# Optimization experiments

Measured on AMD Instinct MI355X. Metric: run time of the kernel, lower is better.

Reference implementation:

```python
import jax, jax.numpy as jnp
import numpy as np

EPS_SN = 1e-12
EPS_BN = 1e-5
NEG_SLOPE = 0.01  # nn.LeakyReLU default


def _l2n(v):
    return v / (jnp.linalg.norm(v) + EPS_SN)


def _sn_weight(w, u, v):
    # one power iteration (as in SpectralNorm._update_u_v), u/v are buffers
    h = w.shape[0]
    W2 = w.reshape(h, -1)
    Wd = jax.lax.stop_gradient(W2)
    v = _l2n(Wd.T @ u)
    u = _l2n(Wd @ v)
    sigma = u @ (W2 @ v)  # gradient flows through W2 only
    return w / sigma


def _conv(x, w, pad):
    return jax.lax.conv_general_dilated(
        x, w, window_strides=(1, 1), padding=[(pad, pad), (pad, pad)],
        dimension_numbers=('NCHW', 'OIHW', 'NCHW'))


def _bn(x, scale, bias):
    # BatchNorm2d in training mode: biased batch stats over (B,H,W)
    mean = x.mean(axis=(0, 2, 3), keepdims=True)
    var = x.var(axis=(0, 2, 3), keepdims=True)
    xn = (x - mean) * jax.lax.rsqrt(var + EPS_BN)
    return xn * scale[None, :, None, None] + bias[None, :, None, None]


def setup_inputs() -> dict:
    key = jax.random.key(0)
    ks = jax.random.split(key, 16)
    B, C, W, H = 2, 256, 64, 64
    Cq = C // 4
    inp = {
        'x': jax.random.normal(ks[0], (B, C, W, H), jnp.float32),
        'pre': jax.random.normal(ks[1], (B, C, W, H), jnp.float32),
        'mask': (jax.random.uniform(ks[2], (B, 1, W, H)) > 0.5).astype(jnp.float32),
        'q_w': jax.random.normal(ks[3], (Cq, C, 1, 1), jnp.float32) * 0.02,
        'gamma': jnp.array(0.5, jnp.float32),
        'alpha': jnp.array(0.5, jnp.float32),
        'bn1_s': jnp.ones((2 * C,), jnp.float32),
        'bn1_b': jnp.zeros((2 * C,), jnp.float32),
        'c1_w': jax.random.normal(ks[4], (C, 2 * C, 3, 3), jnp.float32) * 0.02,
        'u1': _l2n(jax.random.normal(ks[5], (C,), jnp.float32)),
        'v1': _l2n(jax.random.normal(ks[6], (2 * C * 9,), jnp.float32)),
        'bn2_s': jnp.ones((C,), jnp.float32),
        'bn2_b': jnp.zeros((C,), jnp.float32),
        'c2_w': jax.random.normal(ks[7], (C, C, 3, 3), jnp.float32) * 0.02,
        'u2': _l2n(jax.random.normal(ks[8], (C,), jnp.float32)),
        'v2': _l2n(jax.random.normal(ks[9], (C * 9,), jnp.float32)),
        'by_w': jax.random.normal(ks[10], (C, 2 * C, 1, 1), jnp.float32) * 0.02,
        'u3': _l2n(jax.random.normal(ks[11], (C,), jnp.float32)),
        'v3': _l2n(jax.random.normal(ks[12], (2 * C,), jnp.float32)),
    }
    return inp


def reference(x, pre, mask, q_w, gamma, alpha, bn1_s, bn1_b, c1_w, u1, v1,
              bn2_s, bn2_b, c2_w, u2, v2, by_w, u3, v3):
    B, C, W, H = x.shape
    N = W * H
    q = _conv(x, q_w, 0).reshape(B, -1, N)
    energy = jnp.einsum('bcn,bcm->bnm', q, q)       # B x N x N (query == key)
    attention = jax.nn.softmax(energy, axis=-1)
    val = x.reshape(B, C, N)
    # torch.bmm(value, attention^T): out[b,c,j] = sum_k val[b,c,k] * attn[b,j,k]
    out = jnp.einsum('bck,bjk->bcj', val, attention).reshape(B, C, W, H)
    out = gamma * out + x

    context_flow = jnp.einsum('bck,bjk->bcj', pre.reshape(B, -1, N), attention)
    context_flow = context_flow.reshape(B, -1, W, H)
    context_flow = alpha * (1 - mask) * context_flow + mask * pre

    y = jnp.concatenate([out, context_flow], axis=1)  # B x 2C x W x H
    # ResBlock(2C -> C, hidden C, BatchNorm, spectral norm, sample_type='none')
    h = jax.nn.leaky_relu(_bn(y, bn1_s, bn1_b), NEG_SLOPE)
    h = _conv(h, _sn_weight(c1_w, u1, v1), 1)
    h = jax.nn.leaky_relu(_bn(h, bn2_s, bn2_b), NEG_SLOPE)
    h = _conv(h, _sn_weight(c2_w, u2, v2), 1)
    sc = _conv(y, _sn_weight(by_w, u3, v3), 0)
    res = h + sc
    return res, attention
```

## Files before the change

### kernel.cpp

```cpp
#include <hip/hip_runtime.h>
#include <cstddef>


typedef __attribute__((ext_vector_type(8))) short bh8;
typedef __attribute__((ext_vector_type(4))) short bh4;
typedef __attribute__((ext_vector_type(4))) float f4;

static __device__ __forceinline__ short f2bf(float f) {
  unsigned u = __float_as_uint(f);
  unsigned r = (u + 0x7fffu + ((u >> 16) & 1u)) >> 16;
  return (short)r;
}
static __device__ __forceinline__ float bf2f(unsigned short s) {
  return __uint_as_float(((unsigned)s) << 16);
}

__device__ __forceinline__ float blk_sum256(float v, float* sm) {
#pragma unroll
  for (int o = 32; o > 0; o >>= 1) v += __shfl_down(v, o, 64);
  __syncthreads();
  if ((threadIdx.x & 63) == 0) sm[threadIdx.x >> 6] = v;
  __syncthreads();
  return sm[0] + sm[1] + sm[2] + sm[3];
}

__device__ __forceinline__ float blk_max256(float v, float* sm) {
#pragma unroll
  for (int o = 32; o > 0; o >>= 1) v = fmaxf(v, __shfl_down(v, o, 64));
  __syncthreads();
  if ((threadIdx.x & 63) == 0) sm[threadIdx.x >> 6] = v;
  __syncthreads();
  return fmaxf(fmaxf(sm[0], sm[1]), fmaxf(sm[2], sm[3]));
}

#define SWCOL(row, col) ((col) ^ ((((row) >> 1) & 3) << 3))

__global__ __launch_bounds__(256) void snA_kernel(
    const float* __restrict__ w1, const float* __restrict__ u1,
    const float* __restrict__ w2, const float* __restrict__ u2,
    const float* __restrict__ w3, const float* __restrict__ u3,
    float* __restrict__ t1, float* __restrict__ t2, float* __restrict__ t3) {
  int g = blockIdx.x * 256 + threadIdx.x;
  const float* W; const float* u; float* t; int K; int j;
  if (g < 4608)      { W = w1; u = u1; t = t1; K = 4608; j = g; }
  else if (g < 6912) { W = w2; u = u2; t = t2; K = 2304; j = g - 4608; }
  else if (g < 7424) { W = w3; u = u3; t = t3; K = 512;  j = g - 6912; }
  else return;
  float a = 0.f;
  for (int i = 0; i < 256; ++i) a += W[(size_t)i * K + j] * u[i];
  t[j] = a;
}

__global__ __launch_bounds__(256) void snN_kernel(
    const float* __restrict__ t1, const float* __restrict__ t2,
    const float* __restrict__ t3, float* __restrict__ invn) {
  __shared__ float red[4];
  const float* t; int K;
  if (blockIdx.x == 0)      { t = t1; K = 4608; }
  else if (blockIdx.x == 1) { t = t2; K = 2304; }
  else                      { t = t3; K = 512;  }
  float ss = 0.f;
  for (int j = threadIdx.x; j < K; j += 256) { float v = t[j]; ss += v * v; }
  ss = blk_sum256(ss, red);
  if (threadIdx.x == 0) invn[blockIdx.x] = 1.0f / (sqrtf(ss) + 1e-12f);
}

__global__ __launch_bounds__(256) void snB_kernel(
    const float* __restrict__ w1, const float* __restrict__ t1,
    const float* __restrict__ w2, const float* __restrict__ t2,
    const float* __restrict__ w3, const float* __restrict__ t3,
    float* __restrict__ st) {
  int blk = blockIdx.x;
  int w = blk >> 6;
  const float* W; const float* t; int K;
  if (w == 0)      { W = w1; t = t1; K = 4608; }
  else if (w == 1) { W = w2; t = t2; K = 2304; }
  else             { W = w3; t = t3; K = 512;  }
  int lane = threadIdx.x & 63, wave = threadIdx.x >> 6;
  int row = (blk & 63) * 4 + wave;
  const float* Wr = W + (size_t)row * K;
  float a = 0.f;
  for (int j = lane; j < K; j += 64) a += Wr[j] * t[j];
#pragma unroll
  for (int o = 32; o > 0; o >>= 1) a += __shfl_down(a, o, 64);
  if (lane == 0) st[w * 256 + row] = a;
}

__global__ __launch_bounds__(256) void snC_kernel(
    const float* __restrict__ st, const float* __restrict__ invn,
    float* __restrict__ inv_sig) {
  __shared__ float red[4];
  int w = blockIdx.x;
  float v = st[w * 256 + threadIdx.x];
  float ss = blk_sum256(v * v, red);
  if (threadIdx.x == 0) {
    float in = invn[w];
    float s2 = in * in * ss;
    float sn = in * sqrtf(ss);
    float sigma = s2 / (sn + 1e-12f);
    inv_sig[w] = 1.0f / sigma;
  }
}

__global__ __launch_bounds__(256) void cast_xp_kernel(
    const float* __restrict__ x, const float* __restrict__ pre,
    unsigned short* __restrict__ xb, unsigned short* __restrict__ pb) {
  int i = blockIdx.x * 256 + threadIdx.x;
  const float* s = blockIdx.y ? pre : x;
  unsigned short* d = blockIdx.y ? pb : xb;
  float4 v0 = ((const float4*)s)[i * 2];
  float4 v1 = ((const float4*)s)[i * 2 + 1];
  bh8 o = { f2bf(v0.x), f2bf(v0.y), f2bf(v0.z), f2bf(v0.w),
            f2bf(v1.x), f2bf(v1.y), f2bf(v1.z), f2bf(v1.w) };
  *(bh8*)&d[(size_t)i * 8] = o;
}

__global__ __launch_bounds__(256) void transpose_w_kernel(
    const float* __restrict__ src, unsigned short* __restrict__ dst, int Cin) {
  int i = blockIdx.x * 256 + threadIdx.x;
  int ciin = i & 31;
  int co = (i >> 5) & 255;
  int rest = i >> 13;
  int nchunk = Cin >> 5;
  int cc = rest % nchunk;
  int t = rest / nchunk;
  int ci = (cc << 5) + ciin;
  dst[i] = (unsigned short)f2bf(src[((size_t)co * Cin + ci) * 9 + t]);
}

__global__ __launch_bounds__(256) void cast_w3_kernel(
    const float* __restrict__ src, unsigned short* __restrict__ dst) {
  int i = blockIdx.x * 256 + threadIdx.x;
  float4 v0 = ((const float4*)src)[i * 2];
  float4 v1 = ((const float4*)src)[i * 2 + 1];
  bh8 o = { f2bf(v0.x), f2bf(v0.y), f2bf(v0.z), f2bf(v0.w),
            f2bf(v1.x), f2bf(v1.y), f2bf(v1.z), f2bf(v1.w) };
  *(bh8*)&dst[(size_t)i * 8] = o;
}

__global__ __launch_bounds__(256) void qconv_kernel(
    const float* __restrict__ x, const float* __restrict__ qw, float* __restrict__ q) {
  int gid = blockIdx.x;
  int ntile = gid & 15;
  int cq = (gid >> 4) & 63;
  int b = gid >> 10;
  int n = (ntile << 8) + threadIdx.x;
  const float* xb = x + ((size_t)b << 20) + n;
  const float* wr = qw + cq * 256;
  float acc = 0.f;
#pragma unroll 8
  for (int c = 0; c < 256; ++c) acc += wr[c] * xb[(size_t)c << 12];
  q[(((size_t)(b * 64 + cq)) << 12) + n] = acc;
}

__global__ __launch_bounds__(256) void qtrans_kernel(
    const float* __restrict__ q, unsigned short* __restrict__ qt) {
  int b = blockIdx.y;
  int n0 = blockIdx.x * 64;
  __shared__ float t[64][65];
  int tid = threadIdx.x;
  int col = tid & 63, krow = tid >> 6;
#pragma unroll
  for (int p = 0; p < 16; ++p) {
    int k = p * 4 + krow;
    t[k][col] = q[(((size_t)(b * 64 + k)) << 12) + n0 + col];
  }
  __syncthreads();
#pragma unroll
  for (int p = 0; p < 16; ++p) {
    int r = p * 4 + krow;
    qt[(((size_t)(b * 4096 + n0 + r)) << 6) + col] = (unsigned short)f2bf(t[col][r]);
  }
}

__global__ __launch_bounds__(256, 4) void energy_mfma_kernel(
    const unsigned short* __restrict__ qt, float* __restrict__ att) {
  int b = blockIdx.z;
  int n0 = blockIdx.x << 7;
  int m0 = blockIdx.y << 7;
  __shared__ short Qn[128 * 64];
  __shared__ short Qm[128 * 64];
  int tid = threadIdx.x;
  int wave = tid >> 6, lane = tid & 63;
  int ln = lane & 15, qd = lane >> 4;
  int wy = wave >> 1, wx = wave & 1;
  int g = tid & 7, row0 = tid >> 3;
#pragma unroll
  for (int it = 0; it < 4; ++it) {
    int r = row0 + it * 32;
    int colb = ((g ^ (r & 7)) << 3);
    *(bh8*)&Qn[(r << 6) + colb] =
        *(const bh8*)&qt[((size_t)(b * 4096 + n0 + r) << 6) + (g << 3)];
    *(bh8*)&Qm[(r << 6) + colb] =
        *(const bh8*)&qt[((size_t)(b * 4096 + m0 + r) << 6) + (g << 3)];
  }
  __syncthreads();
  f4 z = {0.f, 0.f, 0.f, 0.f};
  f4 acc[4][4];
#pragma unroll
  for (int i = 0; i < 4; ++i)
#pragma unroll
    for (int j = 0; j < 4; ++j) acc[i][j] = z;
#pragma unroll
  for (int kc = 0; kc < 2; ++kc) {
    bh8 am[4];
#pragma unroll
    for (int j = 0; j < 4; ++j) {
      int row = wx * 64 + j * 16 + ln;
      int colb = (((qd + (kc << 2)) ^ (row & 7)) << 3);
      am[j] = *(const bh8*)&Qm[(row << 6) + colb];
    }
#pragma unroll
    for (int i = 0; i < 4; ++i) {
      int row = wy * 64 + i * 16 + ln;
      int colb = (((qd + (kc << 2)) ^ (row & 7)) << 3);
      bh8 an = *(const bh8*)&Qn[(row << 6) + colb];
#pragma unroll
      for (int j = 0; j < 4; ++j)
        acc[i][j] = __builtin_amdgcn_mfma_f32_16x16x32_bf16(an, am[j], acc[i][j], 0, 0, 0);
    }
  }
  size_t base = ((size_t)b << 24);
#pragma unroll
  for (int i = 0; i < 4; ++i) {
    int n = n0 + wy * 64 + i * 16 + qd * 4;
#pragma unroll
    for (int j = 0; j < 4; ++j) {
      int m = m0 + wx * 64 + j * 16 + ln;
#pragma unroll
      for (int r = 0; r < 4; ++r)
        att[base + (((size_t)(n + r)) << 12) + m] = acc[i][j][r];
    }
  }
}

__global__ __launch_bounds__(256) void softmax_kernel(float* __restrict__ att) {
  __shared__ float red[4];
  size_t row = blockIdx.x;
  float4* rp4 = (float4*)(att + (row << 12));
  int tid = threadIdx.x;
  float4 v[4];
#pragma unroll
  for (int i = 0; i < 4; ++i) v[i] = rp4[tid + (i << 8)];
  float mx = -INFINITY;
#pragma unroll
  for (int i = 0; i < 4; ++i)
    mx = fmaxf(mx, fmaxf(fmaxf(v[i].x, v[i].y), fmaxf(v[i].z, v[i].w)));
  mx = blk_max256(mx, red);
  float s = 0.f;
#pragma unroll
  for (int i = 0; i < 4; ++i) {
    v[i].x = __expf(v[i].x - mx); v[i].y = __expf(v[i].y - mx);
    v[i].z = __expf(v[i].z - mx); v[i].w = __expf(v[i].w - mx);
    s += v[i].x + v[i].y + v[i].z + v[i].w;
  }
  s = blk_sum256(s, red);
  float inv = 1.0f / s;
#pragma unroll
  for (int i = 0; i < 4; ++i) {
    v[i].x *= inv; v[i].y *= inv; v[i].z *= inv; v[i].w *= inv;
    rp4[tid + (i << 8)] = v[i];
  }
}

__global__ __launch_bounds__(256, 2) void outcf_mfma_kernel(
    const unsigned short* __restrict__ xb, const unsigned short* __restrict__ pb,
    const float* __restrict__ x, const float* __restrict__ pre,
    const float* __restrict__ att, const float* __restrict__ mask,
    const float* __restrict__ gamma_p, const float* __restrict__ alpha_p,
    unsigned short* __restrict__ y_t) {
  int b = blockIdx.z;
  int c0 = blockIdx.y * 64;
  int j0 = blockIdx.x * 64;
  __shared__ short smem[12 * 64 * 32];
  int tid = threadIdx.x;
  int wave = tid >> 6, lane = tid & 63;
  short* Xs = smem + wave * (3 * 2048);
  short* Ps = Xs + 2048;
  short* As = Ps + 2048;
  int ln = lane & 15, qd = lane >> 4;
  f4 z = {0.f, 0.f, 0.f, 0.f};
  f4 accO[4][4], accC[4][4];
#pragma unroll
  for (int i = 0; i < 4; ++i)
#pragma unroll
    for (int j = 0; j < 4; ++j) { accO[i][j] = z; accC[i][j] = z; }
  int part = lane & 3, r4 = lane >> 2;
  int part8 = lane & 7, r8 = lane >> 3;
  int kb = wave << 10;
  bh8 xr[4], pr[4];
  float4 ar[8];
#pragma unroll
  for (int t2 = 0; t2 < 4; ++t2) {
    int rr = r4 + t2 * 16;
    xr[t2] = *(const bh8*)&xb[((size_t)(b * 256 + c0 + rr) << 12) + kb + part * 8];
    pr[t2] = *(const bh8*)&pb[((size_t)(b * 256 + c0 + rr) << 12) + kb + part * 8];
  }
#pragma unroll
  for (int t2 = 0; t2 < 8; ++t2) {
    int rr = r8 + t2 * 8;
    ar[t2] = *(const float4*)&att[((size_t)b << 24) + ((size_t)(j0 + rr) << 12) + kb + part8 * 4];
  }
  for (int it = 0; it < 32; ++it) {
    int k0 = kb + (it << 5);
#pragma unroll
    for (int t2 = 0; t2 < 4; ++t2) {
      int rr = r4 + t2 * 16;
      int col = SWCOL(rr, part * 8);
      *(bh8*)&Xs[rr * 32 + col] = xr[t2];
      *(bh8*)&Ps[rr * 32 + col] = pr[t2];
    }
#pragma unroll
    for (int t2 = 0; t2 < 8; ++t2) {
      int rr = r8 + t2 * 8;
      int col = SWCOL(rr, part8 * 4);
      float4 v = ar[t2];
      bh4 o = { f2bf(v.x), f2bf(v.y), f2bf(v.z), f2bf(v.w) };
      *(bh4*)&As[rr * 32 + col] = o;
    }
    if (it + 1 < 32) {
      int k1 = k0 + 32;
#pragma unroll
      for (int t2 = 0; t2 < 4; ++t2) {
        int rr = r4 + t2 * 16;
        xr[t2] = *(const bh8*)&xb[((size_t)(b * 256 + c0 + rr) << 12) + k1 + part * 8];
        pr[t2] = *(const bh8*)&pb[((size_t)(b * 256 + c0 + rr) << 12) + k1 + part * 8];
      }
#pragma unroll
      for (int t2 = 0; t2 < 8; ++t2) {
        int rr = r8 + t2 * 8;
        ar[t2] = *(const float4*)&att[((size_t)b << 24) + ((size_t)(j0 + rr) << 12) + k1 + part8 * 4];
      }
    }
    bh8 bf[4];
#pragma unroll
    for (int j = 0; j < 4; ++j) {
      int row = j * 16 + ln;
      bf[j] = *(const bh8*)&As[row * 32 + SWCOL(row, qd * 8)];
    }
#pragma unroll
    for (int i = 0; i < 4; ++i) {
      int row = i * 16 + ln;
      int col = SWCOL(row, qd * 8);
      bh8 ax = *(const bh8*)&Xs[row * 32 + col];
      bh8 ap = *(const bh8*)&Ps[row * 32 + col];
#pragma unroll
      for (int j = 0; j < 4; ++j) {
        accO[i][j] = __builtin_amdgcn_mfma_f32_16x16x32_bf16(ax, bf[j], accO[i][j], 0, 0, 0);
        accC[i][j] = __builtin_amdgcn_mfma_f32_16x16x32_bf16(ap, bf[j], accC[i][j], 0, 0, 0);
      }
    }
  }
  float* red = (float*)smem;
  __syncthreads();
#pragma unroll
  for (int j = 0; j < 4; ++j) {
    if (j == wave) continue;
    int s = wave - (wave > j ? 1 : 0);
#pragma unroll
    for (int i = 0; i < 4; ++i)
      *(f4*)&red[((((j * 3 + s) << 2) + i) << 8) + (lane << 2)] = accO[i][j];
  }
  __syncthreads();
#pragma unroll
  for (int j = 0; j < 4; ++j) {
    if (j != wave) continue;
#pragma unroll
    for (int s = 0; s < 3; ++s)
#pragma unroll
      for (int i = 0; i < 4; ++i) {
        f4 v = *(const f4*)&red[((((j * 3 + s) << 2) + i) << 8) + (lane << 2)];
        accO[i][j][0] += v[0]; accO[i][j][1] += v[1];
        accO[i][j][2] += v[2]; accO[i][j][3] += v[3];
      }
  }
  __syncthreads();
#pragma unroll
  for (int j = 0; j < 4; ++j) {
    if (j == wave) continue;
    int s = wave - (wave > j ? 1 : 0);
#pragma unroll
    for (int i = 0; i < 4; ++i)
      *(f4*)&red[((((j * 3 + s) << 2) + i) << 8) + (lane << 2)] = accC[i][j];
  }
  __syncthreads();
#pragma unroll
  for (int j = 0; j < 4; ++j) {
    if (j != wave) continue;
#pragma unroll
    for (int s = 0; s < 3; ++s)
#pragma unroll
      for (int i = 0; i < 4; ++i) {
        f4 v = *(const f4*)&red[((((j * 3 + s) << 2) + i) << 8) + (lane << 2)];
        accC[i][j][0] += v[0]; accC[i][j][1] += v[1];
        accC[i][j][2] += v[2]; accC[i][j][3] += v[3];
      }
  }
  float g = gamma_p[0], al = alpha_p[0];
#pragma unroll
  for (int j = 0; j < 4; ++j) {
    if (j != wave) continue;
    int jp = j0 + j * 16 + ln;
    float mv = mask[(b << 12) + jp];
#pragma unroll
    for (int i = 0; i < 4; ++i) {
      int cb = c0 + i * 16 + qd * 4;
      bh4 oY, oC;
#pragma unroll
      for (int r = 0; r < 4; ++r) {
        float xo = x[((size_t)(b * 256 + cb + r) << 12) + jp];
        float po = pre[((size_t)(b * 256 + cb + r) << 12) + jp];
        oY[r] = f2bf(g * accO[i][j][r] + xo);
        oC[r] = f2bf(al * (1.f - mv) * accC[i][j][r] + mv * po);
      }
      size_t rowb = ((size_t)b * 4096 + jp) * 512;
      *(bh4*)&y_t[rowb + cb] = oY;
      *(bh4*)&y_t[rowb + 256 + cb] = oC;
    }
  }
}

__global__ __launch_bounds__(256) void bn_part_kernel(
    const void* __restrict__ src, int isbf, int C, int rows_per_slab,
    float* __restrict__ part) {
  int slab = blockIdx.x;
  int r0 = slab * rows_per_slab;
  for (int co = threadIdx.x; co < C; co += 256) {
    float s = 0.f, ss = 0.f;
    if (isbf) {
      const unsigned short* p = (const unsigned short*)src;
      for (int r = 0; r < rows_per_slab; ++r) {
        float v = bf2f(p[(size_t)(r0 + r) * C + co]); s += v; ss += v * v;
      }
    } else {
      const float* p = (const float*)src;
      for (int r = 0; r < rows_per_slab; ++r) {
        float v = p[(size_t)(r0 + r) * C + co]; s += v; ss += v * v;
      }
    }
    part[(size_t)(slab * 2) * C + co] = s;
    part[(size_t)(slab * 2 + 1) * C + co] = ss;
  }
}

__global__ __launch_bounds__(256) void bn_finish_kernel(
    const float* __restrict__ part, int C, int slabs, float inv_count,
    float* __restrict__ mean, float* __restrict__ rstd) {
  for (int co = threadIdx.x; co < C; co += 256) {
    float s = 0.f, ss = 0.f;
    for (int sl = 0; sl < slabs; ++sl) {
      s += part[(size_t)(sl * 2) * C + co];
      ss += part[(size_t)(sl * 2 + 1) * C + co];
    }
    float m = s * inv_count;
    float var = ss * inv_count - m * m;
    mean[co] = m;
    rstd[co] = rsqrtf(var + 1e-5f);
  }
}

__global__ __launch_bounds__(256) void bn_act_bf_kernel(
    const unsigned short* __restrict__ src, unsigned short* __restrict__ dst,
    const float* __restrict__ mean, const float* __restrict__ rstd,
    const float* __restrict__ sc, const float* __restrict__ bi, int Cm1) {
  int i = blockIdx.x * 256 + threadIdx.x;
  int ch = (i * 4) & Cm1;
  bh4 v = *(const bh4*)&src[(size_t)i * 4];
  bh4 o;
#pragma unroll
  for (int e = 0; e < 4; ++e) {
    int c = ch + e;
    float a = rstd[c] * sc[c];
    float bb = bi[c] - mean[c] * a;
    float f = bf2f((unsigned short)v[e]) * a + bb;
    f = f > 0.f ? f : 0.01f * f;
    o[e] = f2bf(f);
  }
  *(bh4*)&dst[(size_t)i * 4] = o;
}

__global__ __launch_bounds__(256) void bn_act_f_kernel(
    const float* __restrict__ src, unsigned short* __restrict__ dst,
    const float* __restrict__ mean, const float* __restrict__ rstd,
    const float* __restrict__ sc, const float* __restrict__ bi, int Cm1) {
  int i = blockIdx.x * 256 + threadIdx.x;
  int ch = (i * 4) & Cm1;
  float4 v = ((const float4*)src)[i];
  float vv[4] = {v.x, v.y, v.z, v.w};
  bh4 o;
#pragma unroll
  for (int e = 0; e < 4; ++e) {
    int c = ch + e;
    float a = rstd[c] * sc[c];
    float bb = bi[c] - mean[c] * a;
    float f = vv[e] * a + bb;
    f = f > 0.f ? f : 0.01f * f;
    o[e] = f2bf(f);
  }
  *(bh4*)&dst[(size_t)i * 4] = o;
}

__global__ __launch_bounds__(256, 2) void conv3x3_mfma_kernel(
    const unsigned short* __restrict__ act_t, const unsigned short* __restrict__ wt,
    const float* __restrict__ inv_sig, int sidx, int Cin, int mode,
    float* __restrict__ out) {
  int b = blockIdx.z;
  int co0 = blockIdx.y * 64;
  int n0 = blockIdx.x * 64;
  __shared__ short smem[4 * 194 * 32];
  int tid = threadIdx.x;
  int wave = tid >> 6, lane = tid & 63;
  short* act_s = smem + wave * (194 * 32);
  int ln = lane & 15, qd = lane >> 4;
  int part = lane & 3, r4 = lane >> 2;
  f4 z = {0.f, 0.f, 0.f, 0.f};
  f4 acc[4][4];
#pragma unroll
  for (int i = 0; i < 4; ++i)
#pragma unroll
    for (int j = 0; j < 4; ++j) acc[i][j] = z;
  bh8 zf = {};
  int nchunk = Cin >> 5;
  int per = nchunk >> 2;
  size_t tstride = (size_t)nchunk * 256 * 32;
  int cc0 = wave * per;
  bh8 sreg[13];
#pragma unroll
  for (int it = 0; it < 13; ++it) {
    int rr = r4 + it * 16;
    bh8 v = {};
    if (rr < 194) {
      int flat = n0 - 65 + rr;
      if ((unsigned)flat < 4096u)
        v = *(const bh8*)&act_t[((size_t)(b * 4096 + flat)) * Cin + (cc0 << 5) + part * 8];
    }
    sreg[it] = v;
  }
  for (int itc = 0; itc < per; ++itc) {
    int cc = cc0 + itc;
#pragma unroll
    for (int it = 0; it < 13; ++it) {
      int rr = r4 + it * 16;
      if (rr < 194)
        *(bh8*)&act_s[rr * 32 + SWCOL(rr, part * 8)] = sreg[it];
    }
    if (itc + 1 < per) {
      int ci0n = (cc + 1) << 5;
#pragma unroll
      for (int it = 0; it < 13; ++it) {
        int rr = r4 + it * 16;
        bh8 v = {};
        if (rr < 194) {
          int flat = n0 - 65 + rr;
          if ((unsigned)flat < 4096u)
            v = *(const bh8*)&act_t[((size_t)(b * 4096 + flat)) * Cin + ci0n + part * 8];
        }
        sreg[it] = v;
      }
    }
    const unsigned short* wb0 = wt + ((size_t)cc * 256) * 32;
    bh8 bwc[4], bwn[4];
#pragma unroll
    for (int j = 0; j < 4; ++j)
      bwc[j] = *(const bh8*)&wb0[(size_t)(co0 + j * 16 + ln) * 32 + qd * 8];
#pragma unroll
    for (int t = 0; t < 9; ++t) {
      if (t < 8) {
        const unsigned short* wbn = wb0 + (size_t)(t + 1) * tstride;
#pragma unroll
        for (int j = 0; j < 4; ++j)
          bwn[j] = *(const bh8*)&wbn[(size_t)(co0 + j * 16 + ln) * 32 + qd * 8];
      }
      int dy = t / 3, dx = t - dy * 3;
      int off = (dy - 1) * 64 + (dx - 1);
#pragma unroll
      for (int i = 0; i < 4; ++i) {
        int px = i * 16 + ln;
        int row = 65 + off + px;
        bh8 a = *(const bh8*)&act_s[row * 32 + SWCOL(row, qd * 8)];
        if (dx == 0 && px == 0) a = zf;
        if (dx == 2 && px == 63) a = zf;
#pragma unroll
        for (int j = 0; j < 4; ++j)
          acc[i][j] = __builtin_amdgcn_mfma_f32_16x16x32_bf16(a, bwc[j], acc[i][j], 0, 0, 0);
      }
      if (t < 8) {
#pragma unroll
        for (int j = 0; j < 4; ++j) bwc[j] = bwn[j];
      }
    }
  }
  float* red = (float*)smem;
  __syncthreads();
#pragma unroll
  for (int j = 0; j < 4; ++j) {
    if (j == wave) continue;
    int s = wave - (wave > j ? 1 : 0);
#pragma unroll
    for (int i = 0; i < 4; ++i)
      *(f4*)&red[((((j * 3 + s) << 2) + i) << 8) + (lane << 2)] = acc[i][j];
  }
  __syncthreads();
#pragma unroll
  for (int j = 0; j < 4; ++j) {
    if (j != wave) continue;
#pragma unroll
    for (int s = 0; s < 3; ++s)
#pragma unroll
      for (int i = 0; i < 4; ++i) {
        f4 v = *(const f4*)&red[((((j * 3 + s) << 2) + i) << 8) + (lane << 2)];
        acc[i][j][0] += v[0]; acc[i][j][1] += v[1];
        acc[i][j][2] += v[2]; acc[i][j][3] += v[3];
      }
  }
  float isg = inv_sig[sidx];
  if (mode == 0) {
#pragma unroll
    for (int j = 0; j < 4; ++j) {
      if (j != wave) continue;
      int co = co0 + j * 16 + ln;
#pragma unroll
      for (int i = 0; i < 4; ++i) {
        int pb = n0 + i * 16 + qd * 4;
#pragma unroll
        for (int r = 0; r < 4; ++r)
          out[((size_t)(b * 4096 + pb + r)) * 256 + co] = acc[i][j][r] * isg;
      }
    }
  } else {
#pragma unroll
    for (int j = 0; j < 4; ++j) {
      if (j != wave) continue;
      int co = co0 + j * 16 + ln;
#pragma unroll
      for (int i = 0; i < 4; ++i) {
        int pb = n0 + i * 16 + qd * 4;
        float4* rp = (float4*)&out[((size_t)(b * 256 + co) << 12) + pb];
        float4 v = *rp;
        v.x += acc[i][j][0] * isg; v.y += acc[i][j][1] * isg;
        v.z += acc[i][j][2] * isg; v.w += acc[i][j][3] * isg;
        *rp = v;
      }
    }
  }
}

__global__ __launch_bounds__(256, 2) void scgemm_mfma_kernel(
    const unsigned short* __restrict__ y_t, const unsigned short* __restrict__ w3b,
    const float* __restrict__ inv_sig, float* __restrict__ res) {
  int b = blockIdx.z;
  int co0 = blockIdx.y * 64;
  int n0 = blockIdx.x * 64;
  __shared__ short smem[24576];
  int tid = threadIdx.x;
  int wave = tid >> 6, lane = tid & 63;
  short* Ys = smem + wave * 2048;
  int ln = lane & 15, qd = lane >> 4;
  int part = lane & 3, r4 = lane >> 2;
  f4 z = {0.f, 0.f, 0.f, 0.f};
  f4 acc[4][4];
#pragma unroll
  for (int i = 0; i < 4; ++i)
#pragma unroll
    for (int j = 0; j < 4; ++j) acc[i][j] = z;
  int kb = wave << 7;
  bh8 ys[4], bwc[4], yn[4], bwn[4];
#pragma unroll
  for (int t2 = 0; t2 < 4; ++t2) {
    int rr = r4 + t2 * 16;
    ys[t2] = *(const bh8*)&y_t[((size_t)(b * 4096 + n0 + rr)) * 512 + kb + part * 8];
  }
#pragma unroll
  for (int j = 0; j < 4; ++j)
    bwc[j] = *(const bh8*)&w3b[((size_t)(co0 + j * 16 + ln)) * 512 + kb + qd * 8];
#pragma unroll
  for (int it = 0; it < 4; ++it) {
    int k0 = kb + (it << 5);
#pragma unroll
    for (int t2 = 0; t2 < 4; ++t2) {
      int rr = r4 + t2 * 16;
      *(bh8*)&Ys[rr * 32 + SWCOL(rr, part * 8)] = ys[t2];
    }
    if (it < 3) {
      int k1 = k0 + 32;
#pragma unroll
      for (int t2 = 0; t2 < 4; ++t2) {
        int rr = r4 + t2 * 16;
        yn[t2] = *(const bh8*)&y_t[((size_t)(b * 4096 + n0 + rr)) * 512 + k1 + part * 8];
      }
#pragma unroll
      for (int j = 0; j < 4; ++j)
        bwn[j] = *(const bh8*)&w3b[((size_t)(co0 + j * 16 + ln)) * 512 + k1 + qd * 8];
    }
#pragma unroll
    for (int i = 0; i < 4; ++i) {
      int row = i * 16 + ln;
      bh8 a = *(const bh8*)&Ys[row * 32 + SWCOL(row, qd * 8)];
#pragma unroll
      for (int j = 0; j < 4; ++j)
        acc[i][j] = __builtin_amdgcn_mfma_f32_16x16x32_bf16(a, bwc[j], acc[i][j], 0, 0, 0);
    }
    if (it < 3) {
#pragma unroll
      for (int t2 = 0; t2 < 4; ++t2) ys[t2] = yn[t2];
#pragma unroll
      for (int j = 0; j < 4; ++j) bwc[j] = bwn[j];
    }
  }
  float* red = (float*)smem;
  __syncthreads();
#pragma unroll
  for (int j = 0; j < 4; ++j) {
    if (j == wave) continue;
    int s = wave - (wave > j ? 1 : 0);
#pragma unroll
    for (int i = 0; i < 4; ++i)
      *(f4*)&red[((((j * 3 + s) << 2) + i) << 8) + (lane << 2)] = acc[i][j];
  }
  __syncthreads();
#pragma unroll
  for (int j = 0; j < 4; ++j) {
    if (j != wave) continue;
#pragma unroll
    for (int s = 0; s < 3; ++s)
#pragma unroll
      for (int i = 0; i < 4; ++i) {
        f4 v = *(const f4*)&red[((((j * 3 + s) << 2) + i) << 8) + (lane << 2)];
        acc[i][j][0] += v[0]; acc[i][j][1] += v[1];
        acc[i][j][2] += v[2]; acc[i][j][3] += v[3];
      }
  }
  float isg = inv_sig[2];
#pragma unroll
  for (int j = 0; j < 4; ++j) {
    if (j != wave) continue;
    int co = co0 + j * 16 + ln;
#pragma unroll
    for (int i = 0; i < 4; ++i) {
      int pb = n0 + i * 16 + qd * 4;
      float4 o;
      o.x = acc[i][j][0] * isg; o.y = acc[i][j][1] * isg;
      o.z = acc[i][j][2] * isg; o.w = acc[i][j][3] * isg;
      *(float4*)&res[((size_t)(b * 256 + co) << 12) + pb] = o;
    }
  }
}

extern "C" void kernel_launch(void* const* d_in, const int* in_sizes, int n_in,
                              void* d_out, int out_size, void* d_ws, size_t ws_size,
                              hipStream_t stream) {
  const float* x     = (const float*)d_in[0];
  const float* pre   = (const float*)d_in[1];
  const float* mask  = (const float*)d_in[2];
  const float* qw    = (const float*)d_in[3];
  const float* gamma = (const float*)d_in[4];
  const float* alpha = (const float*)d_in[5];
  const float* bn1s  = (const float*)d_in[6];
  const float* bn1b  = (const float*)d_in[7];
  const float* c1w   = (const float*)d_in[8];
  const float* u1    = (const float*)d_in[9];
  const float* bn2s  = (const float*)d_in[11];
  const float* bn2b  = (const float*)d_in[12];
  const float* c2w   = (const float*)d_in[13];
  const float* u2    = (const float*)d_in[14];
  const float* byw   = (const float*)d_in[16];
  const float* u3    = (const float*)d_in[17];

  float* res = (float*)d_out;
  float* att = res + (size_t)2 * 256 * 4096;

  char* W = (char*)d_ws;
  float* inv_sig = (float*)(W + 0);
  float* mean1   = (float*)(W + 64);
  float* rstd1   = (float*)(W + 2112);
  float* mean2   = (float*)(W + 4160);
  float* rstd2   = (float*)(W + 5184);
  float* part    = (float*)(W + 8192);
  float* q       = (float*)(W + 270336);
  unsigned short* x_bf = (unsigned short*)(W + 2367488);
  unsigned short* p_bf = (unsigned short*)(W + 6561792);
  unsigned short* y_t  = (unsigned short*)(W + 10756096);
  unsigned short* act1 = (unsigned short*)(W + 19144704);
  float* h1_t          = (float*)(W + 27533312);
  unsigned short* act2 = (unsigned short*)(W + 35921920);
  unsigned short* w1t  = (unsigned short*)(W + 40116224);
  unsigned short* w2t  = (unsigned short*)(W + 42475520);
  unsigned short* w3b  = (unsigned short*)(W + 43655168);
  float* t1      = (float*)(W + 43917312);
  float* t2      = (float*)(W + 43935744);
  float* t3      = (float*)(W + 43944960);
  float* invn    = (float*)(W + 43947008);
  float* st      = (float*)(W + 43947072);
  unsigned short* qt = (unsigned short*)(W + 19144704);

  hipLaunchKernelGGL(snA_kernel, dim3(29), dim3(256), 0, stream,
                     c1w, u1, c2w, u2, byw, u3, t1, t2, t3);
  hipLaunchKernelGGL(snN_kernel, dim3(3), dim3(256), 0, stream, t1, t2, t3, invn);
  hipLaunchKernelGGL(snB_kernel, dim3(192), dim3(256), 0, stream,
                     c1w, t1, c2w, t2, byw, t3, st);
  hipLaunchKernelGGL(snC_kernel, dim3(3), dim3(256), 0, stream, st, invn, inv_sig);
  hipLaunchKernelGGL(cast_xp_kernel, dim3(1024, 2), dim3(256), 0, stream, x, pre, x_bf, p_bf);
  hipLaunchKernelGGL(transpose_w_kernel, dim3(4608), dim3(256), 0, stream, c1w, w1t, 512);
  hipLaunchKernelGGL(transpose_w_kernel, dim3(2304), dim3(256), 0, stream, c2w, w2t, 256);
  hipLaunchKernelGGL(cast_w3_kernel, dim3(64), dim3(256), 0, stream, byw, w3b);
  hipLaunchKernelGGL(qconv_kernel, dim3(2048), dim3(256), 0, stream, x, qw, q);
  hipLaunchKernelGGL(qtrans_kernel, dim3(64, 2), dim3(256), 0, stream, q, qt);
  hipLaunchKernelGGL(energy_mfma_kernel, dim3(32, 32, 2), dim3(256), 0, stream, qt, att);
  hipLaunchKernelGGL(softmax_kernel, dim3(8192), dim3(256), 0, stream, att);
  hipLaunchKernelGGL(outcf_mfma_kernel, dim3(64, 4, 2), dim3(256), 0, stream,
                     x_bf, p_bf, x, pre, att, mask, gamma, alpha, y_t);
  hipLaunchKernelGGL(bn_part_kernel, dim3(64), dim3(256), 0, stream,
                     (const void*)y_t, 1, 512, 128, part);
  hipLaunchKernelGGL(bn_finish_kernel, dim3(1), dim3(256), 0, stream,
                     part, 512, 64, 1.0f / 8192.0f, mean1, rstd1);
  hipLaunchKernelGGL(bn_act_bf_kernel, dim3(8192), dim3(256), 0, stream,
                     y_t, act1, mean1, rstd1, bn1s, bn1b, 511);
  hipLaunchKernelGGL(conv3x3_mfma_kernel, dim3(64, 4, 2), dim3(256), 0, stream,
                     act1, w1t, inv_sig, 0, 512, 0, h1_t);
  hipLaunchKernelGGL(bn_part_kernel, dim3(64), dim3(256), 0, stream,
                     (const void*)h1_t, 0, 256, 128, part);
  hipLaunchKernelGGL(bn_finish_kernel, dim3(1), dim3(256), 0, stream,
                     part, 256, 64, 1.0f / 8192.0f, mean2, rstd2);
  hipLaunchKernelGGL(bn_act_f_kernel, dim3(2048), dim3(256), 0, stream,
                     h1_t, act2, mean2, rstd2, bn2s, bn2b, 255);
  hipLaunchKernelGGL(scgemm_mfma_kernel, dim3(64, 4, 2), dim3(256), 0, stream,
                     y_t, w3b, inv_sig, res);
  hipLaunchKernelGGL(conv3x3_mfma_kernel, dim3(64, 4, 2), dim3(256), 0, stream,
                     act2, w2t, inv_sig, 1, 256, 1, res);
}
```

Baseline: 607.6 us.

## Fuse q conv and transpose into MFMA GEMM; restructure outcf pipelining and block order

Replaces the scalar fp32 1x1 query conv plus separate transpose kernel with a single bf16 MFMA GEMM that reads the bf16 copy of x and writes the transposed q directly. This removes one launch and the fp32 q round trip. In the attention-value kernel, attention tiles are now converted to bf16 at load time, and the loop is unrolled by two with double register buffers so global loads overlap MFMA work. The grid is also flattened so that blocks sharing an attention row tile are scheduled together, which should improve L2 reuse. Risks are higher register pressure and bf16 rounding of the q weights.

```diff
diff --git a/kernel.cpp b/kernel.cpp
--- a/kernel.cpp
+++ b/kernel.cpp
@@ -138,38 +138,98 @@
   *(bh8*)&dst[(size_t)i * 8] = o;
 }
 
-__global__ __launch_bounds__(256) void qconv_kernel(
-    const float* __restrict__ x, const float* __restrict__ qw, float* __restrict__ q) {
-  int gid = blockIdx.x;
-  int ntile = gid & 15;
-  int cq = (gid >> 4) & 63;
-  int b = gid >> 10;
-  int n = (ntile << 8) + threadIdx.x;
-  const float* xb = x + ((size_t)b << 20) + n;
-  const float* wr = qw + cq * 256;
-  float acc = 0.f;
-#pragma unroll 8
-  for (int c = 0; c < 256; ++c) acc += wr[c] * xb[(size_t)c << 12];
-  q[(((size_t)(b * 64 + cq)) << 12) + n] = acc;
-}
-
-__global__ __launch_bounds__(256) void qtrans_kernel(
-    const float* __restrict__ q, unsigned short* __restrict__ qt) {
+__global__ __launch_bounds__(256, 2) void qgemm_kernel(
+    const unsigned short* __restrict__ xb, const float* __restrict__ qw,
+    unsigned short* __restrict__ qt) {
   int b = blockIdx.y;
   int n0 = blockIdx.x * 64;
-  __shared__ float t[64][65];
+  __shared__ short smem[24576];
   int tid = threadIdx.x;
-  int col = tid & 63, krow = tid >> 6;
-#pragma unroll
-  for (int p = 0; p < 16; ++p) {
-    int k = p * 4 + krow;
-    t[k][col] = q[(((size_t)(b * 64 + k)) << 12) + n0 + col];
-  }
-  __syncthreads();
-#pragma unroll
-  for (int p = 0; p < 16; ++p) {
-    int r = p * 4 + krow;
-    qt[(((size_t)(b * 4096 + n0 + r)) << 6) + col] = (unsigned short)f2bf(t[col][r]);
+  int wave = tid >> 6, lane = tid & 63;
+  short* Wt = smem + wave * 4096;
+  short* Xt = Wt + 2048;
+  int ln = lane & 15, qd = lane >> 4;
+  int part = lane & 3, r4 = lane >> 2;
+  int cl = lane >> 1, ng = lane & 1;
+  f4 z = {0.f, 0.f, 0.f, 0.f};
+  f4 acc[4][4];
+#pragma unroll
+  for (int i = 0; i < 4; ++i)
+#pragma unroll
+    for (int j = 0; j < 4; ++j) acc[i][j] = z;
+#pragma unroll
+  for (int kc = 0; kc < 2; ++kc) {
+    int cc = wave * 2 + kc;
+    int c0c = cc << 5;
+#pragma unroll
+    for (int t2 = 0; t2 < 4; ++t2) {
+      int rr = r4 + t2 * 16;
+      const float* wp = &qw[rr * 256 + c0c + part * 8];
+      float4 v0 = *(const float4*)wp;
+      float4 v1 = *(const float4*)(wp + 4);
+      bh8 o = { f2bf(v0.x), f2bf(v0.y), f2bf(v0.z), f2bf(v0.w),
+                f2bf(v1.x), f2bf(v1.y), f2bf(v1.z), f2bf(v1.w) };
+      *(bh8*)&Wt[rr * 32 + SWCOL(rr, part * 8)] = o;
+    }
+#pragma unroll
+    for (int it = 0; it < 4; ++it) {
+      int gg = ng + it * 2;
+      bh8 v = *(const bh8*)&xb[((size_t)(b * 256 + c0c + cl) << 12) + n0 + gg * 8];
+#pragma unroll
+      for (int e = 0; e < 8; ++e) {
+        int nl = gg * 8 + e;
+        Xt[nl * 32 + (cl ^ (((nl >> 1) & 3) << 3))] = v[e];
+      }
+    }
+    bh8 bw[4];
+#pragma unroll
+    for (int j = 0; j < 4; ++j) {
+      int row = j * 16 + ln;
+      bw[j] = *(const bh8*)&Wt[row * 32 + SWCOL(row, qd * 8)];
+    }
+#pragma unroll
+    for (int i = 0; i < 4; ++i) {
+      int row = i * 16 + ln;
+      bh8 a = *(const bh8*)&Xt[row * 32 + SWCOL(row, qd * 8)];
+#pragma unroll
+      for (int j = 0; j < 4; ++j)
+        acc[i][j] = __builtin_amdgcn_mfma_f32_16x16x32_bf16(a, bw[j], acc[i][j], 0, 0, 0);
+    }
+  }
+  float* red = (float*)smem;
+  __syncthreads();
+#pragma unroll
+  for (int j = 0; j < 4; ++j) {
+    if (j == wave) continue;
+    int s = wave - (wave > j ? 1 : 0);
+#pragma unroll
+    for (int i = 0; i < 4; ++i)
+      *(f4*)&red[((((j * 3 + s) << 2) + i) << 8) + (lane << 2)] = acc[i][j];
+  }
+  __syncthreads();
+#pragma unroll
+  for (int j = 0; j < 4; ++j) {
+    if (j != wave) continue;
+#pragma unroll
+    for (int s = 0; s < 3; ++s)
+#pragma unroll
+      for (int i = 0; i < 4; ++i) {
+        f4 v = *(const f4*)&red[((((j * 3 + s) << 2) + i) << 8) + (lane << 2)];
+        acc[i][j][0] += v[0]; acc[i][j][1] += v[1];
+        acc[i][j][2] += v[2]; acc[i][j][3] += v[3];
+      }
+  }
+#pragma unroll
+  for (int j = 0; j < 4; ++j) {
+    if (j != wave) continue;
+#pragma unroll
+    for (int i = 0; i < 4; ++i) {
+      int n = n0 + i * 16 + qd * 4;
+#pragma unroll
+      for (int r = 0; r < 4; ++r)
+        qt[((size_t)(b * 4096 + n + r) << 6) + j * 16 + ln] =
+            (unsigned short)f2bf(acc[i][j][r]);
+    }
   }
 }
 
@@ -269,9 +329,11 @@
     const float* __restrict__ att, const float* __restrict__ mask,
     const float* __restrict__ gamma_p, const float* __restrict__ alpha_p,
     unsigned short* __restrict__ y_t) {
-  int b = blockIdx.z;
-  int c0 = blockIdx.y * 64;
-  int j0 = blockIdx.x * 64;
+  int bid = blockIdx.x;
+  int grp = bid & 7;
+  int b = grp >> 2;
+  int c0 = (grp & 3) * 64;
+  int j0 = (bid >> 3) * 64;
   __shared__ short smem[12 * 64 * 32];
   int tid = threadIdx.x;
   int wave = tid >> 6, lane = tid & 63;
@@ -288,8 +350,9 @@
   int part = lane & 3, r4 = lane >> 2;
   int part8 = lane & 7, r8 = lane >> 3;
   int kb = wave << 10;
+  size_t abase = ((size_t)b << 24);
   bh8 xr[4], pr[4];
-  float4 ar[8];
+  bh4 arA[8], arB[8];
 #pragma unroll
   for (int t2 = 0; t2 < 4; ++t2) {
     int rr = r4 + t2 * 16;
@@ -299,10 +362,19 @@
 #pragma unroll
   for (int t2 = 0; t2 < 8; ++t2) {
     int rr = r8 + t2 * 8;
-    ar[t2] = *(const float4*)&att[((size_t)b << 24) + ((size_t)(j0 + rr) << 12) + kb + part8 * 4];
-  }
-  for (int it = 0; it < 32; ++it) {
-    int k0 = kb + (it << 5);
+    float4 v = *(const float4*)&att[abase + ((size_t)(j0 + rr) << 12) + kb + part8 * 4];
+    bh4 o = { f2bf(v.x), f2bf(v.y), f2bf(v.z), f2bf(v.w) };
+    arA[t2] = o;
+  }
+#pragma unroll
+  for (int t2 = 0; t2 < 8; ++t2) {
+    int rr = r8 + t2 * 8;
+    float4 v = *(const float4*)&att[abase + ((size_t)(j0 + rr) << 12) + kb + 32 + part8 * 4];
+    bh4 o = { f2bf(v.x), f2bf(v.y), f2bf(v.z), f2bf(v.w) };
+    arB[t2] = o;
+  }
+  for (int it = 0; it < 32; it += 2) {
+    int kA = kb + (it << 5);
 #pragma unroll
     for (int t2 = 0; t2 < 4; ++t2) {
       int rr = r4 + t2 * 16;
@@ -313,41 +385,97 @@
 #pragma unroll
     for (int t2 = 0; t2 < 8; ++t2) {
       int rr = r8 + t2 * 8;
-      int col = SWCOL(rr, part8 * 4);
-      float4 v = ar[t2];
-      bh4 o = { f2bf(v.x), f2bf(v.y), f2bf(v.z), f2bf(v.w) };
-      *(bh4*)&As[rr * 32 + col] = o;
-    }
-    if (it + 1 < 32) {
-      int k1 = k0 + 32;
+      *(bh4*)&As[rr * 32 + SWCOL(rr, part8 * 4)] = arA[t2];
+    }
+    {
+      int k1 = kA + 32;
 #pragma unroll
       for (int t2 = 0; t2 < 4; ++t2) {
         int rr = r4 + t2 * 16;
         xr[t2] = *(const bh8*)&xb[((size_t)(b * 256 + c0 + rr) << 12) + k1 + part * 8];
         pr[t2] = *(const bh8*)&pb[((size_t)(b * 256 + c0 + rr) << 12) + k1 + part * 8];
       }
+    }
+    if (it + 2 < 32) {
+      int k2 = kA + 64;
 #pragma unroll
       for (int t2 = 0; t2 < 8; ++t2) {
         int rr = r8 + t2 * 8;
-        ar[t2] = *(const float4*)&att[((size_t)b << 24) + ((size_t)(j0 + rr) << 12) + k1 + part8 * 4];
-      }
-    }
-    bh8 bf[4];
-#pragma unroll
-    for (int j = 0; j < 4; ++j) {
-      int row = j * 16 + ln;
-      bf[j] = *(const bh8*)&As[row * 32 + SWCOL(row, qd * 8)];
-    }
-#pragma unroll
-    for (int i = 0; i < 4; ++i) {
-      int row = i * 16 + ln;
-      int col = SWCOL(row, qd * 8);
-      bh8 ax = *(const bh8*)&Xs[row * 32 + col];
-      bh8 ap = *(const bh8*)&Ps[row * 32 + col];
+        float4 v = *(const float4*)&att[abase + ((size_t)(j0 + rr) << 12) + k2 + part8 * 4];
+        bh4 o = { f2bf(v.x), f2bf(v.y), f2bf(v.z), f2bf(v.w) };
+        arA[t2] = o;
+      }
+    }
+    {
+      bh8 bf[4];
 #pragma unroll
       for (int j = 0; j < 4; ++j) {
-        accO[i][j] = __builtin_amdgcn_mfma_f32_16x16x32_bf16(ax, bf[j], accO[i][j], 0, 0, 0);
-        accC[i][j] = __builtin_amdgcn_mfma_f32_16x16x32_bf16(ap, bf[j], accC[i][j], 0, 0, 0);
+        int row = j * 16 + ln;
+        bf[j] = *(const bh8*)&As[row * 32 + SWCOL(row, qd * 8)];
+      }
+#pragma unroll
+      for (int i = 0; i < 4; ++i) {
+        int row = i * 16 + ln;
+        int col = SWCOL(row, qd * 8);
+        bh8 ax = *(const bh8*)&Xs[row * 32 + col];
+        bh8 ap = *(const bh8*)&Ps[row * 32 + col];
+#pragma unroll
+        for (int j = 0; j < 4; ++j) {
+          accO[i][j] = __builtin_amdgcn_mfma_f32_16x16x32_bf16(ax, bf[j], accO[i][j], 0, 0, 0);
+          accC[i][j] = __builtin_amdgcn_mfma_f32_16x16x32_bf16(ap, bf[j], accC[i][j], 0, 0, 0);
+        }
+      }
+    }
+    int kB = kA + 32;
+#pragma unroll
+    for (int t2 = 0; t2 < 4; ++t2) {
+      int rr = r4 + t2 * 16;
+      int col = SWCOL(rr, part * 8);
+      *(bh8*)&Xs[rr * 32 + col] = xr[t2];
+      *(bh8*)&Ps[rr * 32 + col] = pr[t2];
+    }
+#pragma unroll
+    for (int t2 = 0; t2 < 8; ++t2) {
+      int rr = r8 + t2 * 8;
+      *(bh4*)&As[rr * 32 + SWCOL(rr, part8 * 4)] = arB[t2];
+    }
+    if (it + 2 < 32) {
+      int k1 = kB + 32;
+#pragma unroll
+      for (int t2 = 0; t2 < 4; ++t2) {
+        int rr = r4 + t2 * 16;
+        xr[t2] = *(const bh8*)&xb[((size_t)(b * 256 + c0 + rr) << 12) + k1 + part * 8];
+        pr[t2] = *(const bh8*)&pb[((size_t)(b * 256 + c0 + rr) << 12) + k1 + part * 8];
+      }
+    }
+    if (it + 3 < 32) {
+      int k2 = kB + 64;
+#pragma unroll
+      for (int t2 = 0; t2 < 8; ++t2) {
+        int rr = r8 + t2 * 8;
+        float4 v = *(const float4*)&att[abase + ((size_t)(j0 + rr) << 12) + k2 + part8 * 4];
+        bh4 o = { f2bf(v.x), f2bf(v.y), f2bf(v.z), f2bf(v.w) };
+        arB[t2] = o;
+      }
+    }
+    {
+      bh8 bf[4];
+#pragma unroll
+      for (int j = 0; j < 4; ++j) {
+        int row = j * 16 + ln;
+        bf[j] = *(const bh8*)&As[row * 32 + SWCOL(row, qd * 8)];
+      }
+#pragma unroll
+      for (int i = 0; i < 4; ++i) {
+        int row = i * 16 + ln;
+        int col = SWCOL(row, qd * 8);
+        bh8 ax = *(const bh8*)&Xs[row * 32 + col];
+        bh8 ap = *(const bh8*)&Ps[row * 32 + col];
+#pragma unroll
+        for (int j = 0; j < 4; ++j) {
+          accO[i][j] = __builtin_amdgcn_mfma_f32_16x16x32_bf16(ax, bf[j], accO[i][j], 0, 0, 0);
+          accC[i][j] = __builtin_amdgcn_mfma_f32_16x16x32_bf16(ap, bf[j], accC[i][j], 0, 0, 0);
+        }
       }
     }
   }
@@ -776,7 +904,6 @@
   float* mean2   = (float*)(W + 4160);
   float* rstd2   = (float*)(W + 5184);
   float* part    = (float*)(W + 8192);
-  float* q       = (float*)(W + 270336);
   unsigned short* x_bf = (unsigned short*)(W + 2367488);
   unsigned short* p_bf = (unsigned short*)(W + 6561792);
   unsigned short* y_t  = (unsigned short*)(W + 10756096);
@@ -803,11 +930,10 @@
   hipLaunchKernelGGL(transpose_w_kernel, dim3(4608), dim3(256), 0, stream, c1w, w1t, 512);
   hipLaunchKernelGGL(transpose_w_kernel, dim3(2304), dim3(256), 0, stream, c2w, w2t, 256);
   hipLaunchKernelGGL(cast_w3_kernel, dim3(64), dim3(256), 0, stream, byw, w3b);
-  hipLaunchKernelGGL(qconv_kernel, dim3(2048), dim3(256), 0, stream, x, qw, q);
-  hipLaunchKernelGGL(qtrans_kernel, dim3(64, 2), dim3(256), 0, stream, q, qt);
+  hipLaunchKernelGGL(qgemm_kernel, dim3(64, 2), dim3(256), 0, stream, x_bf, qw, qt);
   hipLaunchKernelGGL(energy_mfma_kernel, dim3(32, 32, 2), dim3(256), 0, stream, qt, att);
   hipLaunchKernelGGL(softmax_kernel, dim3(8192), dim3(256), 0, stream, att);
-  hipLaunchKernelGGL(outcf_mfma_kernel, dim3(64, 4, 2), dim3(256), 0, stream,
+  hipLaunchKernelGGL(outcf_mfma_kernel, dim3(512), dim3(256), 0, stream,
                      x_bf, p_bf, x, pre, att, mask, gamma, alpha, y_t);
   hipLaunchKernelGGL(bn_part_kernel, dim3(64), dim3(256), 0, stream,
                      (const void*)y_t, 1, 512, 128, part);
```

After: 718.7 us. 1.18x slower.
